# Kernel optimization log

Measured on AMD Instinct MI355X. Metric: run time of the kernel, lower is better.

## Reference

```python
import jax, jax.numpy as jnp
import numpy as np

N, E, IN_DIM, HID, OUT, H = 50000, 800000, 128, 96, 96, 4
C1, C2 = HID // H, OUT // H
EPS = 1e-5

def _lin(key, out_f, in_f):
    kw, kb = jax.random.split(key)
    s = 1.0 / np.sqrt(in_f)
    W = jax.random.uniform(kw, (out_f, in_f), jnp.float32, -s, s)
    b = jax.random.uniform(kb, (out_f,), jnp.float32, -s, s)
    return W, b

def setup_inputs() -> dict:
    key = jax.random.key(0)
    ks = jax.random.split(key, 16)
    x = jax.random.normal(ks[0], (N, IN_DIM), jnp.float32)
    edge_index = jax.random.randint(ks[1], (2, E), 0, N, jnp.int64)
    Wq1, bq1 = _lin(ks[2], HID, IN_DIM)
    Wk1, bk1 = _lin(ks[3], HID, IN_DIM)
    Wv1, bv1 = _lin(ks[4], HID, IN_DIM)
    Ws1, bs1 = _lin(ks[5], HID, IN_DIM)
    Wb1 = _lin(ks[6], 1, 3 * HID)[0]
    Wq2, bq2 = _lin(ks[7], OUT, HID)
    Wk2, bk2 = _lin(ks[8], OUT, HID)
    Wv2, bv2 = _lin(ks[9], OUT, HID)
    Ws2, bs2 = _lin(ks[10], OUT, HID)
    Wb2 = _lin(ks[11], 1, 3 * OUT)[0]
    gamma = jnp.ones((OUT,), jnp.float32)
    beta = jnp.zeros((OUT,), jnp.float32)
    return dict(x=x, edge_index=edge_index, Wq1=Wq1, bq1=bq1, Wk1=Wk1, bk1=bk1,
                Wv1=Wv1, bv1=bv1, Ws1=Ws1, bs1=bs1, Wb1=Wb1,
                Wq2=Wq2, bq2=bq2, Wk2=Wk2, bk2=bk2, Wv2=Wv2, bv2=bv2,
                Ws2=Ws2, bs2=bs2, Wb2=Wb2, gamma=gamma, beta=beta)

def transformer_conv(x, src, dst, Wq, bq, Wk, bk, Wv, bv, Ws, bs, Wb, heads, ch):
    n = x.shape[0]
    q = (x @ Wq.T + bq).reshape(n, heads, ch)
    k = (x @ Wk.T + bk).reshape(n, heads, ch)
    v = (x @ Wv.T + bv).reshape(n, heads, ch)
    # per-edge attention logits [E, H]
    alpha = jnp.einsum('ehc,ehc->eh', q[dst], k[src]) / jnp.sqrt(jnp.float32(ch))
    amax = jax.ops.segment_max(alpha, dst, num_segments=n)
    a = jnp.exp(alpha - amax[dst])
    denom = jax.ops.segment_sum(a, dst, num_segments=n)
    a = a / denom[dst]
    msg = v[src] * a[:, :, None]                       # [E, H, C]
    out = jax.ops.segment_sum(msg, dst, num_segments=n).reshape(n, heads * ch)
    x_r = x @ Ws.T + bs                                # root/skip transform
    g = jax.nn.sigmoid(jnp.concatenate([out, x_r, out - x_r], -1) @ Wb.T)
    return g * x_r + (1.0 - g) * out

def reference(x, edge_index, Wq1, bq1, Wk1, bk1, Wv1, bv1, Ws1, bs1, Wb1,
              Wq2, bq2, Wk2, bk2, Wv2, bv2, Ws2, bs2, Wb2, gamma, beta):
    src, dst = edge_index[0], edge_index[1]
    h = transformer_conv(x, src, dst, Wq1, bq1, Wk1, bk1, Wv1, bv1, Ws1, bs1, Wb1, H, C1)
    h = jax.nn.gelu(h, approximate=False)
    h = transformer_conv(h, src, dst, Wq2, bq2, Wk2, bk2, Wv2, bv2, Ws2, bs2, Wb2, H, C2)
    mu = jnp.mean(h, axis=-1, keepdims=True)
    var = jnp.mean(jnp.square(h - mu), axis=-1, keepdims=True)
    return (h - mu) / jnp.sqrt(var + EPS) * gamma + beta
```

## Files before the change

kernel.cpp:

```cpp
#include <hip/hip_runtime.h>
#include <hip/hip_bf16.h>
#include <hip/hip_fp16.h>
#include <math.h>

constexpr int NN = 50000;
constexpr int EE = 800000;
constexpr int SCAN_NB = (NN + 255) / 256;

typedef short v8s __attribute__((ext_vector_type(8)));
typedef float v4f __attribute__((ext_vector_type(4)));

__device__ __forceinline__ short f2b(float f){
  __hip_bfloat16 h = __float2bfloat16(f);
  return *reinterpret_cast<short*>(&h);
}
__device__ __forceinline__ __half2 u2h2(unsigned int u){
  union { unsigned int u; __half2 h; } c; c.u = u; return c.h;
}

__global__ void zero_i32(int* __restrict__ p, int n){
  int i = blockIdx.x * blockDim.x + threadIdx.x;
  if (i < n) p[i] = 0;
}

__global__ void hist_kernel(const int* __restrict__ ei, int* __restrict__ deg){
  int e = blockIdx.x * blockDim.x + threadIdx.x;
  if (e < EE) atomicAdd(&deg[ei[EE + e]], 1);
}

__global__ __launch_bounds__(256) void partial_sum_kernel(const int* __restrict__ deg,
                                                          int* __restrict__ psum){
  int b = blockIdx.x, tid = threadIdx.x, lane = tid & 63, wv = tid >> 6;
  int i = b * 256 + tid;
  int v = (i < NN) ? deg[i] : 0;
  #pragma unroll
  for (int m = 1; m < 64; m <<= 1) v += __shfl_xor(v, m);
  __shared__ int ws[4];
  if (lane == 0) ws[wv] = v;
  __syncthreads();
  if (tid == 0) psum[b] = ws[0] + ws[1] + ws[2] + ws[3];
}

__global__ __launch_bounds__(256) void scan_partials_kernel(int* __restrict__ psum){
  int tid = threadIdx.x, lane = tid & 63, wv = tid >> 6;
  int own = (tid < SCAN_NB) ? psum[tid] : 0;
  int v = own;
  #pragma unroll
  for (int off = 1; off < 64; off <<= 1){
    int t = __shfl_up(v, off);
    if (lane >= off) v += t;
  }
  __shared__ int ws[4];
  if (lane == 63) ws[wv] = v;
  __syncthreads();
  int add = 0;
  #pragma unroll
  for (int w = 0; w < 4; w++) if (w < wv) add += ws[w];
  if (tid < SCAN_NB) psum[tid] = v + add - own;
}

__global__ __launch_bounds__(256) void final_scan_kernel(const int* __restrict__ deg,
                                                         const int* __restrict__ psum,
                                                         int* __restrict__ row_ptr,
                                                         int* __restrict__ cursor){
  int b = blockIdx.x, tid = threadIdx.x, lane = tid & 63, wv = tid >> 6;
  int i = b * 256 + tid;
  int d = (i < NN) ? deg[i] : 0;
  int v = d;
  #pragma unroll
  for (int off = 1; off < 64; off <<= 1){
    int t = __shfl_up(v, off);
    if (lane >= off) v += t;
  }
  __shared__ int ws[4];
  if (lane == 63) ws[wv] = v;
  __syncthreads();
  int add = psum[b];
  #pragma unroll
  for (int w = 0; w < 4; w++) if (w < wv) add += ws[w];
  if (i < NN){
    row_ptr[i + 1] = add + v;
    cursor[i]      = add + v - d;
  }
  if (i == 0) row_ptr[0] = 0;
}

__global__ void fill_kernel(const int* __restrict__ ei, int* __restrict__ cursor,
                            int* __restrict__ col_src){
  int e = blockIdx.x * blockDim.x + threadIdx.x;
  if (e < EE){
    int src = ei[e], dst = ei[EE + e];
    int pos = atomicAdd(&cursor[dst], 1);
    col_src[pos] = src;
  }
}

__global__ void pack_kernel(const float* __restrict__ Wq, const float* __restrict__ bq,
                            const float* __restrict__ Wk, const float* __restrict__ bk,
                            const float* __restrict__ Wv, const float* __restrict__ bv,
                            const float* __restrict__ Ws, const float* __restrict__ bs,
                            short* __restrict__ Wcat, float* __restrict__ bcat, int K){
  int c = blockIdx.x;
  int which = c / 96, r = c % 96;
  const float* Wsel = which == 0 ? Wq : which == 1 ? Wk : which == 2 ? Wv : Ws;
  const float* bsel = which == 0 ? bq : which == 1 ? bk : which == 2 ? bv : bs;
  for (int k = threadIdx.x; k < K; k += blockDim.x)
    Wcat[(size_t)c * K + k] = f2b(Wsel[(size_t)r * K + k]);
  if (threadIdx.x == 0) bcat[c] = bsel[r];
}

template<int K, bool AF32>
__global__ __launch_bounds__(512) void gemm_kernel(const void* __restrict__ Ain,
                                                   const short* __restrict__ Wcat,
                                                   const float* __restrict__ bcat,
                                                   float* __restrict__ qs,
                                                   __half* __restrict__ kvb,
                                                   int M){
  constexpr int KP = K + 8;
  constexpr int UNITS = K / 8;
  __shared__ __attribute__((aligned(16))) short As[256 * KP];
  __shared__ __attribute__((aligned(16))) short Bs[128 * KP];
  const int tid = threadIdx.x;
  const int rt = blockIdx.x * 256, ct = blockIdx.y * 128;

  #pragma unroll
  for (int it = 0; it < (256 * UNITS) / 512; ++it){
    int li = it * 512 + tid;
    int row = li / UNITS, u = li % UNITS;
    int grow = min(rt + row, M - 1);
    if constexpr (AF32){
      const float* A = (const float*)Ain;
      float4 a0 = *(const float4*)(A + (size_t)grow * K + u * 8);
      float4 a1 = *(const float4*)(A + (size_t)grow * K + u * 8 + 4);
      v8s o;
      o[0] = f2b(a0.x); o[1] = f2b(a0.y); o[2] = f2b(a0.z); o[3] = f2b(a0.w);
      o[4] = f2b(a1.x); o[5] = f2b(a1.y); o[6] = f2b(a1.z); o[7] = f2b(a1.w);
      *(v8s*)&As[row * KP + u * 8] = o;
    } else {
      const short* A = (const short*)Ain;
      *(v8s*)&As[row * KP + u * 8] = *(const v8s*)(A + (size_t)grow * K + u * 8);
    }
  }
  #pragma unroll
  for (int it = 0; it < (128 * UNITS) / 512; ++it){
    int li = it * 512 + tid;
    int row = li / UNITS, u = li % UNITS;
    int gcol = ct + row;
    *(v8s*)&Bs[row * KP + u * 8] = *(const v8s*)(Wcat + (size_t)gcol * K + u * 8);
  }
  __syncthreads();

  const int lane = tid & 63;
  const int wid  = tid >> 6;
  const int wm = wid >> 1, wn = wid & 1;
  const int fr = lane & 15, fk = lane >> 4;

  v4f acc[4][4];
  #pragma unroll
  for (int i = 0; i < 4; i++)
    #pragma unroll
    for (int j = 0; j < 4; j++) acc[i][j] = (v4f){0.f, 0.f, 0.f, 0.f};

  #pragma unroll
  for (int ks = 0; ks < K / 32; ++ks){
    const int kofs = ks * 32 + fk * 8;
    v8s a[4], b[4];
    #pragma unroll
    for (int i = 0; i < 4; i++)
      a[i] = *(const v8s*)&As[(wm * 64 + i * 16 + fr) * KP + kofs];
    #pragma unroll
    for (int j = 0; j < 4; j++)
      b[j] = *(const v8s*)&Bs[(wn * 64 + j * 16 + fr) * KP + kofs];
    #pragma unroll
    for (int i = 0; i < 4; i++)
      #pragma unroll
      for (int j = 0; j < 4; j++)
        acc[i][j] = __builtin_amdgcn_mfma_f32_16x16x32_bf16(a[i], b[j], acc[i][j], 0, 0, 0);
  }

  #pragma unroll
  for (int i = 0; i < 4; i++){
    #pragma unroll
    for (int j = 0; j < 4; j++){
      const int gcol = ct + wn * 64 + j * 16 + fr;
      const float bias = bcat[gcol];
      #pragma unroll
      for (int r = 0; r < 4; r++){
        const int grow = rt + wm * 64 + i * 16 + fk * 4 + r;
        if (grow < M){
          float val = acc[i][j][r] + bias;
          if (gcol < 96)       qs[(size_t)grow * 192 + gcol] = val;
          else if (gcol < 192) kvb[(size_t)grow * 192 + (gcol - 96)] = __float2half(val);
          else if (gcol < 288) kvb[(size_t)grow * 192 + 96 + (gcol - 192)] = __float2half(val);
          else                 qs[(size_t)grow * 192 + 96 + (gcol - 288)] = val;
        }
      }
    }
  }
}

__global__ __launch_bounds__(256) void attn_kernel(
    const float* __restrict__ qs, const __half* __restrict__ kv,
    const int* __restrict__ row_ptr, const int* __restrict__ col_src,
    const float* __restrict__ Wb, const float* __restrict__ gamma,
    const float* __restrict__ beta, float* __restrict__ outp,
    short* __restrict__ h1b, int mode){
  const int lane = threadIdx.x & 63;
  const int wid  = threadIdx.x >> 6;
  const int n = blockIdx.x * 4 + wid;
  if (n >= NN) return;
  const int h_a = lane & 3;
  const int g_a = lane >> 2;
  const int l_v = lane & 15;
  const int vg  = lane >> 4;
  const int h_v = l_v >> 2;

  __half2 qh[12];
  {
    const float* qrow = qs + (size_t)n * 192 + h_a * 24;
    #pragma unroll
    for (int i = 0; i < 12; i++)
      qh[i] = __floats2half2_rn(qrow[2 * i], qrow[2 * i + 1]);
  }
  const int rs = row_ptr[n], re = row_ptr[n + 1];
  float m = -INFINITY, s = 0.f;
  float acc[6] = {0.f, 0.f, 0.f, 0.f, 0.f, 0.f};

  for (int cb = rs; cb < re; cb += 16){
    const int cn = re - cb;
    int srcv = col_src[cb + min(g_a, cn - 1)];
    int sb[4];
    #pragma unroll
    for (int st = 0; st < 4; st++)
      sb[st] = __shfl(srcv, 4 * min(st * 4 + vg, cn - 1));
    unsigned int vd[4][3];
    #pragma unroll
    for (int st = 0; st < 4; st++){
      const unsigned int* vp =
        (const unsigned int*)((const char*)kv + (size_t)sb[st] * 384 + 192 + 12 * l_v);
      vd[st][0] = vp[0]; vd[st][1] = vp[1]; vd[st][2] = vp[2];
    }
    const uint4* kp = (const uint4*)((const char*)kv + (size_t)srcv * 384 + h_a * 48);
    uint4 u0 = kp[0], u1 = kp[1], u2 = kp[2];
    __half2 d0 = __floats2half2_rn(0.f, 0.f), d1 = d0;
    d0 = __hfma2(qh[0],  u2h2(u0.x), d0); d1 = __hfma2(qh[1],  u2h2(u0.y), d1);
    d0 = __hfma2(qh[2],  u2h2(u0.z), d0); d1 = __hfma2(qh[3],  u2h2(u0.w), d1);
    d0 = __hfma2(qh[4],  u2h2(u1.x), d0); d1 = __hfma2(qh[5],  u2h2(u1.y), d1);
    d0 = __hfma2(qh[6],  u2h2(u1.z), d0); d1 = __hfma2(qh[7],  u2h2(u1.w), d1);
    d0 = __hfma2(qh[8],  u2h2(u2.x), d0); d1 = __hfma2(qh[9],  u2h2(u2.y), d1);
    d0 = __hfma2(qh[10], u2h2(u2.z), d0); d1 = __hfma2(qh[11], u2h2(u2.w), d1);
    float dot = __low2float(d0) + __high2float(d0) + __low2float(d1) + __high2float(d1);
    float al = (g_a < cn) ? dot * 0.2041241452319315f : -INFINITY;

    float cm = al;
    cm = fmaxf(cm, __shfl_xor(cm, 4));
    cm = fmaxf(cm, __shfl_xor(cm, 8));
    cm = fmaxf(cm, __shfl_xor(cm, 16));
    cm = fmaxf(cm, __shfl_xor(cm, 32));
    float nm = fmaxf(m, cm);
    float r  = __expf(m - nm);
    float e  = __expf(al - nm);
    float cs = e;
    cs += __shfl_xor(cs, 4);
    cs += __shfl_xor(cs, 8);
    cs += __shfl_xor(cs, 16);
    cs += __shfl_xor(cs, 32);
    s = s * r + cs;
    m = nm;

    float rv = __shfl(r, h_v);
    __half2 ch0 = __floats2half2_rn(0.f, 0.f), ch1 = ch0, ch2 = ch0;
    #pragma unroll
    for (int st = 0; st < 4; st++){
      int eidx = st * 4 + vg;
      float w = __shfl(e, 4 * min(eidx, cn - 1) + h_v);
      if (eidx >= cn) w = 0.f;
      __half2 w2 = __float2half2_rn(w);
      ch0 = __hfma2(w2, u2h2(vd[st][0]), ch0);
      ch1 = __hfma2(w2, u2h2(vd[st][1]), ch1);
      ch2 = __hfma2(w2, u2h2(vd[st][2]), ch2);
    }
    acc[0] = fmaf(acc[0], rv, __low2float(ch0));
    acc[1] = fmaf(acc[1], rv, __high2float(ch0));
    acc[2] = fmaf(acc[2], rv, __low2float(ch1));
    acc[3] = fmaf(acc[3], rv, __high2float(ch1));
    acc[4] = fmaf(acc[4], rv, __low2float(ch2));
    acc[5] = fmaf(acc[5], rv, __high2float(ch2));
  }

  #pragma unroll
  for (int i = 0; i < 6; i++){
    acc[i] += __shfl_xor(acc[i], 16);
    acc[i] += __shfl_xor(acc[i], 32);
  }
  float sv  = __shfl(s, h_v);
  float inv = (re > rs) ? 1.0f / sv : 0.f;
  float o[6], xr[6];
  #pragma unroll
  for (int i = 0; i < 6; i++) o[i] = acc[i] * inv;
  const float* xrp = qs + (size_t)n * 192 + 96 + 6 * l_v;
  #pragma unroll
  for (int i = 0; i < 6; i++) xr[i] = xrp[i];

  float p = 0.f;
  #pragma unroll
  for (int i = 0; i < 6; i++){
    int f = 6 * l_v + i;
    p += Wb[f] * o[i] + Wb[96 + f] * xr[i] + Wb[192 + f] * (o[i] - xr[i]);
  }
  p += __shfl_xor(p, 1);
  p += __shfl_xor(p, 2);
  p += __shfl_xor(p, 4);
  p += __shfl_xor(p, 8);
  float g = 1.0f / (1.0f + __expf(-p));
  float y[6];
  #pragma unroll
  for (int i = 0; i < 6; i++) y[i] = g * xr[i] + (1.0f - g) * o[i];

  if (mode == 0){
    #pragma unroll
    for (int i = 0; i < 6; i++)
      y[i] = 0.5f * y[i] * (1.0f + erff(y[i] * 0.7071067811865475f));
    if (vg == 0){
      short* op = h1b + (size_t)n * 96 + 6 * l_v;
      #pragma unroll
      for (int i = 0; i < 6; i++) op[i] = f2b(y[i]);
    }
  } else {
    float ssum = y[0] + y[1] + y[2] + y[3] + y[4] + y[5];
    ssum += __shfl_xor(ssum, 1);
    ssum += __shfl_xor(ssum, 2);
    ssum += __shfl_xor(ssum, 4);
    ssum += __shfl_xor(ssum, 8);
    float mu = ssum * (1.0f / 96.0f);
    float vsum = 0.f;
    #pragma unroll
    for (int i = 0; i < 6; i++){ float d = y[i] - mu; vsum += d * d; }
    vsum += __shfl_xor(vsum, 1);
    vsum += __shfl_xor(vsum, 2);
    vsum += __shfl_xor(vsum, 4);
    vsum += __shfl_xor(vsum, 8);
    float invs = rsqrtf(vsum * (1.0f / 96.0f) + 1e-5f);
    if (vg == 0){
      float* op = outp + (size_t)n * 96 + 6 * l_v;
      #pragma unroll
      for (int i = 0; i < 6; i++){
        int f = 6 * l_v + i;
        op[i] = (y[i] - mu) * invs * gamma[f] + beta[f];
      }
    }
  }
}

extern "C" void kernel_launch(void* const* d_in, const int* in_sizes, int n_in,
                              void* d_out, int out_size, void* d_ws, size_t ws_size,
                              hipStream_t stream){
  const float* x    = (const float*)d_in[0];
  const int*   ei   = (const int*)d_in[1];
  const float* Wq1  = (const float*)d_in[2];
  const float* bq1  = (const float*)d_in[3];
  const float* Wk1  = (const float*)d_in[4];
  const float* bk1  = (const float*)d_in[5];
  const float* Wv1  = (const float*)d_in[6];
  const float* bv1  = (const float*)d_in[7];
  const float* Ws1  = (const float*)d_in[8];
  const float* bs1  = (const float*)d_in[9];
  const float* Wb1  = (const float*)d_in[10];
  const float* Wq2  = (const float*)d_in[11];
  const float* bq2  = (const float*)d_in[12];
  const float* Wk2  = (const float*)d_in[13];
  const float* bk2  = (const float*)d_in[14];
  const float* Wv2  = (const float*)d_in[15];
  const float* bv2  = (const float*)d_in[16];
  const float* Ws2  = (const float*)d_in[17];
  const float* bs2  = (const float*)d_in[18];
  const float* Wb2  = (const float*)d_in[19];
  const float* gamma = (const float*)d_in[20];
  const float* beta  = (const float*)d_in[21];
  float* out = (float*)d_out;

  char* ws = (char*)d_ws;
  size_t off = 0;
  auto take = [&](size_t b) -> void* {
    void* p = ws + off;
    off += (b + 255) & ~(size_t)255;
    return p;
  };
  float* qs            = (float*)take((size_t)NN * 192 * 4);
  __half* kvb          = (__half*)take((size_t)NN * 192 * 2);
  short* h1b           = (short*)take((size_t)NN * 96 * 2);
  short* Wcat          = (short*)take((size_t)384 * 128 * 2);
  float* bcat          = (float*)take(384 * 4);
  int* deg             = (int*)take((size_t)NN * 4);
  int* cursor          = (int*)take((size_t)NN * 4);
  int* row_ptr         = (int*)take((size_t)(NN + 1) * 4);
  int* col_src         = (int*)take((size_t)EE * 4);
  int* psum            = (int*)take((size_t)SCAN_NB * 4);

  zero_i32<<<(NN + 255) / 256, 256, 0, stream>>>(deg, NN);
  hist_kernel<<<(EE + 255) / 256, 256, 0, stream>>>(ei, deg);
  partial_sum_kernel<<<SCAN_NB, 256, 0, stream>>>(deg, psum);
  scan_partials_kernel<<<1, 256, 0, stream>>>(psum);
  final_scan_kernel<<<SCAN_NB, 256, 0, stream>>>(deg, psum, row_ptr, cursor);
  fill_kernel<<<(EE + 255) / 256, 256, 0, stream>>>(ei, cursor, col_src);

  dim3 gg((NN + 255) / 256, 3);
  pack_kernel<<<384, 128, 0, stream>>>(Wq1, bq1, Wk1, bk1, Wv1, bv1, Ws1, bs1, Wcat, bcat, 128);
  gemm_kernel<128, true><<<gg, 512, 0, stream>>>(x, Wcat, bcat, qs, kvb, NN);
  attn_kernel<<<(NN + 3) / 4, 256, 0, stream>>>(qs, kvb, row_ptr, col_src, Wb1,
                                                nullptr, nullptr, nullptr, h1b, 0);
  pack_kernel<<<384, 128, 0, stream>>>(Wq2, bq2, Wk2, bk2, Wv2, bv2, Ws2, bs2, Wcat, bcat, 96);
  gemm_kernel<96, false><<<gg, 512, 0, stream>>>(h1b, Wcat, bcat, qs, kvb, NN);
  attn_kernel<<<(NN + 3) / 4, 256, 0, stream>>>(qs, kvb, row_ptr, col_src, Wb2,
                                                gamma, beta, out, nullptr, 1);
}
```

Before: 294.2 us.

## Double-buffer edge gathers and use persistent grid-stride waves in attention

The attention kernel now loads up to 64 source indices at once and software-pipelines the K/V gathers. The next 16-edge chunk is prefetched into a second register set while the current chunk is computed, to hide gather latency. Waves are made persistent with a fixed 2048-block grid striding over nodes, and the zeroing kernel is swapped for hipMemsetAsync. The double buffers raise register pressure and can lower occupancy, and the fixed grid may leave load imbalance across waves.

```diff
diff --git a/kernel.cpp b/kernel.cpp
--- a/kernel.cpp
+++ b/kernel.cpp
@@ -16,11 +16,6 @@
 }
 __device__ __forceinline__ __half2 u2h2(unsigned int u){
   union { unsigned int u; __half2 h; } c; c.u = u; return c.h;
-}
-
-__global__ void zero_i32(int* __restrict__ p, int n){
-  int i = blockIdx.x * blockDim.x + threadIdx.x;
-  if (i < n) p[i] = 0;
 }
 
 __global__ void hist_kernel(const int* __restrict__ ei, int* __restrict__ deg){
@@ -207,146 +202,165 @@
     short* __restrict__ h1b, int mode){
   const int lane = threadIdx.x & 63;
   const int wid  = threadIdx.x >> 6;
-  const int n = blockIdx.x * 4 + wid;
-  if (n >= NN) return;
+  const int gw   = blockIdx.x * 4 + wid;
+  const int nw   = gridDim.x * 4;
   const int h_a = lane & 3;
   const int g_a = lane >> 2;
   const int l_v = lane & 15;
   const int vg  = lane >> 4;
   const int h_v = l_v >> 2;
-
-  __half2 qh[12];
-  {
-    const float* qrow = qs + (size_t)n * 192 + h_a * 24;
-    #pragma unroll
-    for (int i = 0; i < 12; i++)
-      qh[i] = __floats2half2_rn(qrow[2 * i], qrow[2 * i + 1]);
-  }
-  const int rs = row_ptr[n], re = row_ptr[n + 1];
-  float m = -INFINITY, s = 0.f;
-  float acc[6] = {0.f, 0.f, 0.f, 0.f, 0.f, 0.f};
-
-  for (int cb = rs; cb < re; cb += 16){
-    const int cn = re - cb;
-    int srcv = col_src[cb + min(g_a, cn - 1)];
-    int sb[4];
-    #pragma unroll
-    for (int st = 0; st < 4; st++)
-      sb[st] = __shfl(srcv, 4 * min(st * 4 + vg, cn - 1));
-    unsigned int vd[4][3];
-    #pragma unroll
-    for (int st = 0; st < 4; st++){
-      const unsigned int* vp =
-        (const unsigned int*)((const char*)kv + (size_t)sb[st] * 384 + 192 + 12 * l_v);
-      vd[st][0] = vp[0]; vd[st][1] = vp[1]; vd[st][2] = vp[2];
-    }
-    const uint4* kp = (const uint4*)((const char*)kv + (size_t)srcv * 384 + h_a * 48);
-    uint4 u0 = kp[0], u1 = kp[1], u2 = kp[2];
-    __half2 d0 = __floats2half2_rn(0.f, 0.f), d1 = d0;
-    d0 = __hfma2(qh[0],  u2h2(u0.x), d0); d1 = __hfma2(qh[1],  u2h2(u0.y), d1);
-    d0 = __hfma2(qh[2],  u2h2(u0.z), d0); d1 = __hfma2(qh[3],  u2h2(u0.w), d1);
-    d0 = __hfma2(qh[4],  u2h2(u1.x), d0); d1 = __hfma2(qh[5],  u2h2(u1.y), d1);
-    d0 = __hfma2(qh[6],  u2h2(u1.z), d0); d1 = __hfma2(qh[7],  u2h2(u1.w), d1);
-    d0 = __hfma2(qh[8],  u2h2(u2.x), d0); d1 = __hfma2(qh[9],  u2h2(u2.y), d1);
-    d0 = __hfma2(qh[10], u2h2(u2.z), d0); d1 = __hfma2(qh[11], u2h2(u2.w), d1);
-    float dot = __low2float(d0) + __high2float(d0) + __low2float(d1) + __high2float(d1);
-    float al = (g_a < cn) ? dot * 0.2041241452319315f : -INFINITY;
-
-    float cm = al;
-    cm = fmaxf(cm, __shfl_xor(cm, 4));
-    cm = fmaxf(cm, __shfl_xor(cm, 8));
-    cm = fmaxf(cm, __shfl_xor(cm, 16));
-    cm = fmaxf(cm, __shfl_xor(cm, 32));
-    float nm = fmaxf(m, cm);
-    float r  = __expf(m - nm);
-    float e  = __expf(al - nm);
-    float cs = e;
-    cs += __shfl_xor(cs, 4);
-    cs += __shfl_xor(cs, 8);
-    cs += __shfl_xor(cs, 16);
-    cs += __shfl_xor(cs, 32);
-    s = s * r + cs;
-    m = nm;
-
-    float rv = __shfl(r, h_v);
-    __half2 ch0 = __floats2half2_rn(0.f, 0.f), ch1 = ch0, ch2 = ch0;
-    #pragma unroll
-    for (int st = 0; st < 4; st++){
-      int eidx = st * 4 + vg;
-      float w = __shfl(e, 4 * min(eidx, cn - 1) + h_v);
-      if (eidx >= cn) w = 0.f;
-      __half2 w2 = __float2half2_rn(w);
-      ch0 = __hfma2(w2, u2h2(vd[st][0]), ch0);
-      ch1 = __hfma2(w2, u2h2(vd[st][1]), ch1);
-      ch2 = __hfma2(w2, u2h2(vd[st][2]), ch2);
-    }
-    acc[0] = fmaf(acc[0], rv, __low2float(ch0));
-    acc[1] = fmaf(acc[1], rv, __high2float(ch0));
-    acc[2] = fmaf(acc[2], rv, __low2float(ch1));
-    acc[3] = fmaf(acc[3], rv, __high2float(ch1));
-    acc[4] = fmaf(acc[4], rv, __low2float(ch2));
-    acc[5] = fmaf(acc[5], rv, __high2float(ch2));
-  }
-
-  #pragma unroll
-  for (int i = 0; i < 6; i++){
-    acc[i] += __shfl_xor(acc[i], 16);
-    acc[i] += __shfl_xor(acc[i], 32);
-  }
-  float sv  = __shfl(s, h_v);
-  float inv = (re > rs) ? 1.0f / sv : 0.f;
-  float o[6], xr[6];
-  #pragma unroll
-  for (int i = 0; i < 6; i++) o[i] = acc[i] * inv;
-  const float* xrp = qs + (size_t)n * 192 + 96 + 6 * l_v;
-  #pragma unroll
-  for (int i = 0; i < 6; i++) xr[i] = xrp[i];
-
-  float p = 0.f;
-  #pragma unroll
-  for (int i = 0; i < 6; i++){
-    int f = 6 * l_v + i;
-    p += Wb[f] * o[i] + Wb[96 + f] * xr[i] + Wb[192 + f] * (o[i] - xr[i]);
-  }
-  p += __shfl_xor(p, 1);
-  p += __shfl_xor(p, 2);
-  p += __shfl_xor(p, 4);
-  p += __shfl_xor(p, 8);
-  float g = 1.0f / (1.0f + __expf(-p));
-  float y[6];
-  #pragma unroll
-  for (int i = 0; i < 6; i++) y[i] = g * xr[i] + (1.0f - g) * o[i];
-
-  if (mode == 0){
-    #pragma unroll
-    for (int i = 0; i < 6; i++)
-      y[i] = 0.5f * y[i] * (1.0f + erff(y[i] * 0.7071067811865475f));
-    if (vg == 0){
-      short* op = h1b + (size_t)n * 96 + 6 * l_v;
+  const char* kvc = (const char*)kv;
+
+  for (int n = gw; n < NN; n += nw){
+    __half2 qh[12];
+    {
+      const float* qrow = qs + (size_t)n * 192 + h_a * 24;
       #pragma unroll
-      for (int i = 0; i < 6; i++) op[i] = f2b(y[i]);
-    }
-  } else {
-    float ssum = y[0] + y[1] + y[2] + y[3] + y[4] + y[5];
-    ssum += __shfl_xor(ssum, 1);
-    ssum += __shfl_xor(ssum, 2);
-    ssum += __shfl_xor(ssum, 4);
-    ssum += __shfl_xor(ssum, 8);
-    float mu = ssum * (1.0f / 96.0f);
-    float vsum = 0.f;
-    #pragma unroll
-    for (int i = 0; i < 6; i++){ float d = y[i] - mu; vsum += d * d; }
-    vsum += __shfl_xor(vsum, 1);
-    vsum += __shfl_xor(vsum, 2);
-    vsum += __shfl_xor(vsum, 4);
-    vsum += __shfl_xor(vsum, 8);
-    float invs = rsqrtf(vsum * (1.0f / 96.0f) + 1e-5f);
-    if (vg == 0){
-      float* op = outp + (size_t)n * 96 + 6 * l_v;
+      for (int i = 0; i < 12; i++)
+        qh[i] = __floats2half2_rn(qrow[2 * i], qrow[2 * i + 1]);
+    }
+    const int rs = row_ptr[n], re = row_ptr[n + 1];
+    float m = -INFINITY, s = 0.f;
+    float acc[6] = {0.f, 0.f, 0.f, 0.f, 0.f, 0.f};
+
+    for (int wb = rs; wb < re; wb += 64){
+      const int wn = min(64, re - wb);
+      const int srcs = col_src[wb + min(lane, wn - 1)];
+      const int nch = (wn + 15) >> 4;
+      uint4 K0[3], K1[3];
+      unsigned V0[4][3], V1[4][3];
+
+      auto LOADC = [&](int c, uint4* K, unsigned (*V)[3]){
+        int ea = min(16 * c + g_a, wn - 1);
+        int sa = __shfl(srcs, ea);
+        unsigned ko = (unsigned)sa * 384u + (unsigned)(h_a * 48);
+        const uint4* kp = (const uint4*)(kvc + ko);
+        K[0] = kp[0]; K[1] = kp[1]; K[2] = kp[2];
+        #pragma unroll
+        for (int st = 0; st < 4; st++){
+          int ev = min(16 * c + st * 4 + vg, wn - 1);
+          int sv = __shfl(srcs, ev);
+          unsigned vo = (unsigned)sv * 384u + 192u + (unsigned)(12 * l_v);
+          const unsigned* vp = (const unsigned*)(kvc + vo);
+          V[st][0] = vp[0]; V[st][1] = vp[1]; V[st][2] = vp[2];
+        }
+      };
+      auto COMPUTE = [&](int c, const uint4* K, const unsigned (*V)[3]){
+        const int cnt = min(wn - 16 * c, 16);
+        __half2 d0 = __floats2half2_rn(0.f, 0.f), d1 = d0;
+        d0 = __hfma2(qh[0],  u2h2(K[0].x), d0); d1 = __hfma2(qh[1],  u2h2(K[0].y), d1);
+        d0 = __hfma2(qh[2],  u2h2(K[0].z), d0); d1 = __hfma2(qh[3],  u2h2(K[0].w), d1);
+        d0 = __hfma2(qh[4],  u2h2(K[1].x), d0); d1 = __hfma2(qh[5],  u2h2(K[1].y), d1);
+        d0 = __hfma2(qh[6],  u2h2(K[1].z), d0); d1 = __hfma2(qh[7],  u2h2(K[1].w), d1);
+        d0 = __hfma2(qh[8],  u2h2(K[2].x), d0); d1 = __hfma2(qh[9],  u2h2(K[2].y), d1);
+        d0 = __hfma2(qh[10], u2h2(K[2].z), d0); d1 = __hfma2(qh[11], u2h2(K[2].w), d1);
+        float dot = __low2float(d0) + __high2float(d0) + __low2float(d1) + __high2float(d1);
+        float al = (g_a < cnt) ? dot * 0.2041241452319315f : -INFINITY;
+        float cm = al;
+        cm = fmaxf(cm, __shfl_xor(cm, 4));
+        cm = fmaxf(cm, __shfl_xor(cm, 8));
+        cm = fmaxf(cm, __shfl_xor(cm, 16));
+        cm = fmaxf(cm, __shfl_xor(cm, 32));
+        float nm = fmaxf(m, cm);
+        float r  = __expf(m - nm);
+        float e  = __expf(al - nm);
+        float cs = e;
+        cs += __shfl_xor(cs, 4);
+        cs += __shfl_xor(cs, 8);
+        cs += __shfl_xor(cs, 16);
+        cs += __shfl_xor(cs, 32);
+        s = s * r + cs;
+        m = nm;
+        float rv = __shfl(r, h_v);
+        __half2 ch0 = __floats2half2_rn(0.f, 0.f), ch1 = ch0, ch2 = ch0;
+        #pragma unroll
+        for (int st = 0; st < 4; st++){
+          float w = __shfl(e, 4 * (st * 4 + vg) + h_v);
+          __half2 w2 = __float2half2_rn(w);
+          ch0 = __hfma2(w2, u2h2(V[st][0]), ch0);
+          ch1 = __hfma2(w2, u2h2(V[st][1]), ch1);
+          ch2 = __hfma2(w2, u2h2(V[st][2]), ch2);
+        }
+        acc[0] = fmaf(acc[0], rv, __low2float(ch0));
+        acc[1] = fmaf(acc[1], rv, __high2float(ch0));
+        acc[2] = fmaf(acc[2], rv, __low2float(ch1));
+        acc[3] = fmaf(acc[3], rv, __high2float(ch1));
+        acc[4] = fmaf(acc[4], rv, __low2float(ch2));
+        acc[5] = fmaf(acc[5], rv, __high2float(ch2));
+      };
+
+      LOADC(0, K0, V0);
+      int c = 0;
+      while (true){
+        if (c + 1 < nch) LOADC(c + 1, K1, V1);
+        COMPUTE(c, K0, V0);
+        if (++c >= nch) break;
+        if (c + 1 < nch) LOADC(c + 1, K0, V0);
+        COMPUTE(c, K1, V1);
+        if (++c >= nch) break;
+      }
+    }
+
+    #pragma unroll
+    for (int i = 0; i < 6; i++){
+      acc[i] += __shfl_xor(acc[i], 16);
+      acc[i] += __shfl_xor(acc[i], 32);
+    }
+    float sv  = __shfl(s, h_v);
+    float inv = (re > rs) ? 1.0f / sv : 0.f;
+    float o[6], xr[6];
+    #pragma unroll
+    for (int i = 0; i < 6; i++) o[i] = acc[i] * inv;
+    const float* xrp = qs + (size_t)n * 192 + 96 + 6 * l_v;
+    #pragma unroll
+    for (int i = 0; i < 6; i++) xr[i] = xrp[i];
+
+    float p = 0.f;
+    #pragma unroll
+    for (int i = 0; i < 6; i++){
+      int f = 6 * l_v + i;
+      p += Wb[f] * o[i] + Wb[96 + f] * xr[i] + Wb[192 + f] * (o[i] - xr[i]);
+    }
+    p += __shfl_xor(p, 1);
+    p += __shfl_xor(p, 2);
+    p += __shfl_xor(p, 4);
+    p += __shfl_xor(p, 8);
+    float g = 1.0f / (1.0f + __expf(-p));
+    float y[6];
+    #pragma unroll
+    for (int i = 0; i < 6; i++) y[i] = g * xr[i] + (1.0f - g) * o[i];
+
+    if (mode == 0){
       #pragma unroll
-      for (int i = 0; i < 6; i++){
-        int f = 6 * l_v + i;
-        op[i] = (y[i] - mu) * invs * gamma[f] + beta[f];
+      for (int i = 0; i < 6; i++)
+        y[i] = 0.5f * y[i] * (1.0f + erff(y[i] * 0.7071067811865475f));
+      if (vg == 0){
+        short* op = h1b + (size_t)n * 96 + 6 * l_v;
+        #pragma unroll
+        for (int i = 0; i < 6; i++) op[i] = f2b(y[i]);
+      }
+    } else {
+      float ssum = y[0] + y[1] + y[2] + y[3] + y[4] + y[5];
+      ssum += __shfl_xor(ssum, 1);
+      ssum += __shfl_xor(ssum, 2);
+      ssum += __shfl_xor(ssum, 4);
+      ssum += __shfl_xor(ssum, 8);
+      float mu = ssum * (1.0f / 96.0f);
+      float vsum = 0.f;
+      #pragma unroll
+      for (int i = 0; i < 6; i++){ float d = y[i] - mu; vsum += d * d; }
+      vsum += __shfl_xor(vsum, 1);
+      vsum += __shfl_xor(vsum, 2);
+      vsum += __shfl_xor(vsum, 4);
+      vsum += __shfl_xor(vsum, 8);
+      float invs = rsqrtf(vsum * (1.0f / 96.0f) + 1e-5f);
+      if (vg == 0){
+        float* op = outp + (size_t)n * 96 + 6 * l_v;
+        #pragma unroll
+        for (int i = 0; i < 6; i++){
+          int f = 6 * l_v + i;
+          op[i] = (y[i] - mu) * invs * gamma[f] + beta[f];
+        }
       }
     }
   }
@@ -397,7 +411,7 @@
   int* col_src         = (int*)take((size_t)EE * 4);
   int* psum            = (int*)take((size_t)SCAN_NB * 4);
 
-  zero_i32<<<(NN + 255) / 256, 256, 0, stream>>>(deg, NN);
+  hipMemsetAsync(deg, 0, (size_t)NN * 4, stream);
   hist_kernel<<<(EE + 255) / 256, 256, 0, stream>>>(ei, deg);
   partial_sum_kernel<<<SCAN_NB, 256, 0, stream>>>(deg, psum);
   scan_partials_kernel<<<1, 256, 0, stream>>>(psum);
@@ -407,10 +421,10 @@
   dim3 gg((NN + 255) / 256, 3);
   pack_kernel<<<384, 128, 0, stream>>>(Wq1, bq1, Wk1, bk1, Wv1, bv1, Ws1, bs1, Wcat, bcat, 128);
   gemm_kernel<128, true><<<gg, 512, 0, stream>>>(x, Wcat, bcat, qs, kvb, NN);
-  attn_kernel<<<(NN + 3) / 4, 256, 0, stream>>>(qs, kvb, row_ptr, col_src, Wb1,
-                                                nullptr, nullptr, nullptr, h1b, 0);
+  attn_kernel<<<2048, 256, 0, stream>>>(qs, kvb, row_ptr, col_src, Wb1,
+                                        nullptr, nullptr, nullptr, h1b, 0);
   pack_kernel<<<384, 128, 0, stream>>>(Wq2, bq2, Wk2, bk2, Wv2, bv2, Ws2, bs2, Wcat, bcat, 96);
   gemm_kernel<96, false><<<gg, 512, 0, stream>>>(h1b, Wcat, bcat, qs, kvb, NN);
-  attn_kernel<<<(NN + 3) / 4, 256, 0, stream>>>(qs, kvb, row_ptr, col_src, Wb2,
-                                                gamma, beta, out, nullptr, 1);
-}
+  attn_kernel<<<2048, 256, 0, stream>>>(qs, kvb, row_ptr, col_src, Wb2,
+                                        gamma, beta, out, nullptr, 1);
+}
```

After: 327.1 us. 11.2% more time.
